# Kernel optimization log

Measured on AMD Instinct MI355X. Metric: run time of the kernel, lower is better.

Reference implementation:

```python
import jax, jax.numpy as jnp
import numpy as np

GAM1 = 1.0
GAM2 = 1.0
EPS = 0.01
NUM_CLASSES = 10


def setup_inputs() -> dict:
    key = jax.random.key(0)
    k1, k2 = jax.random.split(key)
    m, p = 262144, 64
    embed = jax.random.normal(k1, (m, p), dtype=jnp.float32)
    targets = jax.random.randint(k2, (m,), 0, NUM_CLASSES, dtype=jnp.int64)
    return {"embed": embed, "targets": targets}


def reference(embed, targets):
    m, p = embed.shape
    w = embed.T  # (p, m)
    I = jnp.eye(p, dtype=embed.dtype)

    # Discriminative term: logdet(I + gam1 * p/(m*eps) * w w^T) / 2
    scalar = p / (m * EPS)
    _, ld = jnp.linalg.slogdet(I + GAM1 * scalar * (w @ w.T))
    discrimn = ld / 2.0

    # Compressive term. pi[j] is diag(labels == j), so w @ pi[j] @ w^T is the
    # Gram over class-j columns; compute all class Grams in one einsum instead
    # of materializing (k, m, m).
    onehot = jax.nn.one_hot(targets, NUM_CLASSES, dtype=embed.dtype)  # (m, k)
    trPi = onehot.sum(axis=0) + 1e-8  # (k,) == trace(pi[j]) + 1e-8
    grams = jnp.einsum('pm,mk,qm->kpq', w, onehot, w)  # (k, p, p)
    scalars = p / (trPi * EPS)  # (k,)
    mats = I[None, :, :] + scalars[:, None, None] * grams
    _, lds = jnp.linalg.slogdet(mats)  # (k,)
    compress = jnp.sum(lds * trPi / m) / 2.0

    return GAM2 * (-discrimn) + compress
```

## Files before the change

kernel.cpp:

```cpp
#include <hip/hip_runtime.h>
#include <math.h>

#define NCLS 10
#define CHUNK 4096
#define PDIM 64
#define LDX 72
#define LDE 68

typedef short bf16x8 __attribute__((ext_vector_type(8)));
typedef float f32x4 __attribute__((ext_vector_type(4)));

__device__ __forceinline__ unsigned short bf16rn(float x) {
    unsigned u = __float_as_uint(x);
    return (unsigned short)((u + 0x7FFFu + ((u >> 16) & 1u)) >> 16);
}
__device__ __forceinline__ float bf16f(unsigned short h) {
    return __uint_as_float(((unsigned)h) << 16);
}


__global__ __launch_bounds__(256) void mcr_gram(
    const float4* __restrict__ embed4,
    const int* __restrict__ targets,
    float* __restrict__ gram,
    int* __restrict__ counts,
    int m)
{
    __shared__ unsigned short s_list[CHUNK];
    __shared__ int s_cnt;
    __shared__ unsigned short Xh[PDIM * LDX];
    __shared__ unsigned short Xl[PDIM * LDX];

    const int tid = threadIdx.x;
    const int cls = blockIdx.y;
    const int base = blockIdx.x * CHUNK;
    const int lane = tid & 63;

    if (tid == 0) s_cnt = 0;
    __syncthreads();

    const int lim = (m - base < CHUNK) ? (m - base) : CHUNK;
    for (int i = tid; i < lim; i += 256) {
        const bool match = (targets[base + i] == cls);
        const unsigned long long mk = __ballot(match);
        const int cnt = __popcll(mk);
        int wbase = 0;
        if (lane == 0 && cnt) wbase = atomicAdd(&s_cnt, cnt);
        wbase = __shfl(wbase, 0);
        if (match) {
            const int pre = __popcll(mk & ((1ull << lane) - 1ull));
            s_list[wbase + pre] = (unsigned short)i;
        }
    }
    __syncthreads();
    const int n = s_cnt;
    if (n == 0) return;
    if (tid == 0) atomicAdd(&counts[cls], n);

    const int p  = tid & 31;
    const int qA = tid >> 5;
    const int qB = qA + 8;
    const float4 z4 = make_float4(0.f, 0.f, 0.f, 0.f);

    auto load_step = [&](int s, float4& a00, float4& a01, float4& a10, float4& a11) {
        const int r0 = s * 64 + 2 * p;
        const int r1 = r0 + 1;
        if (r0 < n) {
            const size_t row = (size_t)(base + (int)s_list[r0]) * 16;
            a00 = embed4[row + qA];
            a01 = embed4[row + qB];
        } else { a00 = z4; a01 = z4; }
        if (r1 < n) {
            const size_t row = (size_t)(base + (int)s_list[r1]) * 16;
            a10 = embed4[row + qA];
            a11 = embed4[row + qB];
        } else { a10 = z4; a11 = z4; }
    };

    auto stage_write = [&](const float4& a00, const float4& a01,
                           const float4& a10, const float4& a11) {
#pragma unroll
        for (int half = 0; half < 2; ++half) {
            const float* x0 = half ? (const float*)&a01 : (const float*)&a00;
            const float* x1 = half ? (const float*)&a11 : (const float*)&a10;
            const int qq = half ? qB : qA;
#pragma unroll
            for (int j = 0; j < 4; ++j) {
                const int f = qq * 4 + j;
                const unsigned short h0 = bf16rn(x0[j]);
                const unsigned short h1 = bf16rn(x1[j]);
                const unsigned short l0 = bf16rn(x0[j] - bf16f(h0));
                const unsigned short l1 = bf16rn(x1[j] - bf16f(h1));
                *(unsigned int*)&Xh[f * LDX + 2 * p] = (unsigned)h0 | ((unsigned)h1 << 16);
                *(unsigned int*)&Xl[f * LDX + 2 * p] = (unsigned)l0 | ((unsigned)l1 << 16);
            }
        }
    };

    const int w = tid >> 6;
    const int wr = w >> 1, wc = w & 1;
    const int fb = (lane & 15) * LDX + 8 * (lane >> 4);

    f32x4 acc[4];
#pragma unroll
    for (int i = 0; i < 4; ++i) acc[i] = (f32x4){0.f, 0.f, 0.f, 0.f};

    auto mfma_step = [&]() {
#pragma unroll
        for (int kb = 0; kb < 64; kb += 32) {
            const int t0 = (2 * wr) * 16 * LDX + fb + kb;
            const int t1 = (2 * wr + 1) * 16 * LDX + fb + kb;
            const int u0 = (2 * wc) * 16 * LDX + fb + kb;
            const int u1 = (2 * wc + 1) * 16 * LDX + fb + kb;
            const bf16x8 Ah0 = *(const bf16x8*)&Xh[t0];
            const bf16x8 Ah1 = *(const bf16x8*)&Xh[t1];
            const bf16x8 Al0 = *(const bf16x8*)&Xl[t0];
            const bf16x8 Al1 = *(const bf16x8*)&Xl[t1];
            const bf16x8 Bh0 = *(const bf16x8*)&Xh[u0];
            const bf16x8 Bh1 = *(const bf16x8*)&Xh[u1];
            const bf16x8 Bl0 = *(const bf16x8*)&Xl[u0];
            const bf16x8 Bl1 = *(const bf16x8*)&Xl[u1];

            acc[0] = __builtin_amdgcn_mfma_f32_16x16x32_bf16(Ah0, Bh0, acc[0], 0, 0, 0);
            acc[1] = __builtin_amdgcn_mfma_f32_16x16x32_bf16(Ah0, Bh1, acc[1], 0, 0, 0);
            acc[2] = __builtin_amdgcn_mfma_f32_16x16x32_bf16(Ah1, Bh0, acc[2], 0, 0, 0);
            acc[3] = __builtin_amdgcn_mfma_f32_16x16x32_bf16(Ah1, Bh1, acc[3], 0, 0, 0);

            acc[0] = __builtin_amdgcn_mfma_f32_16x16x32_bf16(Ah0, Bl0, acc[0], 0, 0, 0);
            acc[1] = __builtin_amdgcn_mfma_f32_16x16x32_bf16(Ah0, Bl1, acc[1], 0, 0, 0);
            acc[2] = __builtin_amdgcn_mfma_f32_16x16x32_bf16(Ah1, Bl0, acc[2], 0, 0, 0);
            acc[3] = __builtin_amdgcn_mfma_f32_16x16x32_bf16(Ah1, Bl1, acc[3], 0, 0, 0);

            acc[0] = __builtin_amdgcn_mfma_f32_16x16x32_bf16(Al0, Bh0, acc[0], 0, 0, 0);
            acc[1] = __builtin_amdgcn_mfma_f32_16x16x32_bf16(Al0, Bh1, acc[1], 0, 0, 0);
            acc[2] = __builtin_amdgcn_mfma_f32_16x16x32_bf16(Al1, Bh0, acc[2], 0, 0, 0);
            acc[3] = __builtin_amdgcn_mfma_f32_16x16x32_bf16(Al1, Bh1, acc[3], 0, 0, 0);
        }
    };

    const int nsteps = (n + 63) >> 6;
    float4 A00, A01, A10, A11, B00, B01, B10, B11;
    load_step(0, A00, A01, A10, A11);
    load_step(1, B00, B01, B10, B11);

    for (int s = 0; s < nsteps; ++s) {
        if ((s & 1) == 0) {
            stage_write(A00, A01, A10, A11);
            load_step(s + 2, A00, A01, A10, A11);
        } else {
            stage_write(B00, B01, B10, B11);
            load_step(s + 2, B00, B01, B10, B11);
        }
        __syncthreads();
        mfma_step();
        __syncthreads();
    }

    float* gk = gram + cls * (PDIM * PDIM);
    float* gt = gram + NCLS * (PDIM * PDIM);
#pragma unroll
    for (int i1 = 0; i1 < 2; ++i1)
#pragma unroll
        for (int i2 = 0; i2 < 2; ++i2) {
            const int ar = (2 * wr + i1) * 16 + (lane >> 4) * 4;
            const int b  = (2 * wc + i2) * 16 + (lane & 15);
            const f32x4 v = acc[i1 * 2 + i2];
#pragma unroll
            for (int j = 0; j < 4; ++j) {
                const int a = ar + j;
                if (a <= b) {
                    atomicAdd(&gk[a * PDIM + b], v[j]);
                    atomicAdd(&gt[a * PDIM + b], v[j]);
                }
            }
        }
}

__device__ __forceinline__ float gU(const float* __restrict__ gram, int k, int a, int b) {
    const int lo = a < b ? a : b;
    const int hi = a < b ? b : a;
    return gram[k * (PDIM * PDIM) + lo * PDIM + hi];
}

__global__ __launch_bounds__(256) void mcr_logdet(
    const float* __restrict__ gram,
    const int* __restrict__ counts,
    double* __restrict__ contrib,
    unsigned* __restrict__ ctr,
    float* __restrict__ out,
    int m)
{
    __shared__ float E[PDIM * LDE];
    __shared__ float F[PDIM * LDE];
    __shared__ float H[PDIM * LDE];
    __shared__ float G3[PDIM * LDE];
    __shared__ double s_red[4][7];
    __shared__ double s_alpha, s_beta, s_logs, s_w;

    const int tid = threadIdx.x;
    const int k = blockIdx.x;
    const bool tot = (k == NCLS);

    if (tid < PDIM) {
        double d = (double)gU(gram, k, tid, tid);
#pragma unroll
        for (int off = 32; off > 0; off >>= 1) d += __shfl_down(d, off);
        if (tid == 0) {
            const double trG = d;
            const double denom = tot ? (double)m : ((double)counts[k] + 1e-8);
            const double c = (double)PDIM / (denom * 0.01);
            const double s = 1.0 + c * trG / (double)PDIM;
            s_alpha = c / s;
            s_beta = 1.0 / s - 1.0;
            s_logs = (double)PDIM * log(s);
            s_w = tot ? -0.5 : 0.5 * denom / (double)m;
        }
    }
    __syncthreads();

    const double alpha = s_alpha;
    const double beta = s_beta;
    const int ta = (tid >> 4) << 2;
    const int tb = (tid & 15) << 2;

#pragma unroll
    for (int i = 0; i < 4; ++i) {
        const int a = ta + i;
#pragma unroll
        for (int j = 0; j < 4; ++j) {
            const int b = tb + j;
            double v = alpha * (double)gU(gram, k, a, b);
            if (a == b) v += beta;
            E[a * LDE + b] = (float)v;
        }
    }
    __syncthreads();

    {
        float f[4][4];
#pragma unroll
        for (int i = 0; i < 4; ++i)
#pragma unroll
            for (int j = 0; j < 4; ++j) f[i][j] = 0.0f;
#pragma unroll 4
        for (int t = 0; t < PDIM; ++t) {
            const float4 ea4 = *reinterpret_cast<const float4*>(&E[t * LDE + ta]);
            const float4 eb4 = *reinterpret_cast<const float4*>(&E[t * LDE + tb]);
            const float ea[4] = {ea4.x, ea4.y, ea4.z, ea4.w};
            const float eb[4] = {eb4.x, eb4.y, eb4.z, eb4.w};
#pragma unroll
            for (int i = 0; i < 4; ++i)
#pragma unroll
                for (int j = 0; j < 4; ++j) f[i][j] = fmaf(ea[i], eb[j], f[i][j]);
        }
#pragma unroll
        for (int i = 0; i < 4; ++i)
            *reinterpret_cast<float4*>(&F[(ta + i) * LDE + tb]) =
                make_float4(f[i][0], f[i][1], f[i][2], f[i][3]);
    }
    __syncthreads();

    {
        float h[4][4], g3[4][4];
#pragma unroll
        for (int i = 0; i < 4; ++i)
#pragma unroll
            for (int j = 0; j < 4; ++j) { h[i][j] = 0.0f; g3[i][j] = 0.0f; }
#pragma unroll 4
        for (int t = 0; t < PDIM; ++t) {
            const float4 fa4 = *reinterpret_cast<const float4*>(&F[t * LDE + ta]);
            const float4 fb4 = *reinterpret_cast<const float4*>(&F[t * LDE + tb]);
            const float4 eb4 = *reinterpret_cast<const float4*>(&E[t * LDE + tb]);
            const float fa[4] = {fa4.x, fa4.y, fa4.z, fa4.w};
            const float fb[4] = {fb4.x, fb4.y, fb4.z, fb4.w};
            const float eb[4] = {eb4.x, eb4.y, eb4.z, eb4.w};
#pragma unroll
            for (int i = 0; i < 4; ++i)
#pragma unroll
                for (int j = 0; j < 4; ++j) {
                    h[i][j] = fmaf(fa[i], fb[j], h[i][j]);
                    g3[i][j] = fmaf(fa[i], eb[j], g3[i][j]);
                }
        }
#pragma unroll
        for (int i = 0; i < 4; ++i) {
            *reinterpret_cast<float4*>(&H[(ta + i) * LDE + tb]) =
                make_float4(h[i][0], h[i][1], h[i][2], h[i][3]);
            *reinterpret_cast<float4*>(&G3[(ta + i) * LDE + tb]) =
                make_float4(g3[i][0], g3[i][1], g3[i][2], g3[i][3]);
        }
    }
    __syncthreads();

    double t2 = 0, t3 = 0, t4 = 0, t5 = 0, t6 = 0, t7 = 0, t8 = 0;
#pragma unroll
    for (int i = 0; i < 4; ++i)
#pragma unroll
        for (int j = 0; j < 4; ++j) {
            const int idx = (ta + i) * LDE + tb + j;
            const double e = (double)E[idx];
            const double f = (double)F[idx];
            const double h = (double)H[idx];
            const double g = (double)G3[idx];
            t2 += e * e; t3 += f * e; t4 += f * f;
            t5 += h * e; t6 += h * f; t7 += h * g; t8 += h * h;
        }
#pragma unroll
    for (int off = 32; off > 0; off >>= 1) {
        t2 += __shfl_down(t2, off);
        t3 += __shfl_down(t3, off);
        t4 += __shfl_down(t4, off);
        t5 += __shfl_down(t5, off);
        t6 += __shfl_down(t6, off);
        t7 += __shfl_down(t7, off);
        t8 += __shfl_down(t8, off);
    }
    const int lane = tid & 63;
    const int wid = tid >> 6;
    if (lane == 0) {
        s_red[wid][0] = t2; s_red[wid][1] = t3; s_red[wid][2] = t4;
        s_red[wid][3] = t5; s_red[wid][4] = t6; s_red[wid][5] = t7;
        s_red[wid][6] = t8;
    }
    __syncthreads();
    if (tid == 0) {
        double r[7];
        for (int q = 0; q < 7; ++q) {
            r[q] = 0.0;
            for (int w = 0; w < 4; ++w) r[q] += s_red[w][q];
        }
        const double ld = s_logs
            - r[0] / 2.0 + r[1] / 3.0 - r[2] / 4.0 + r[3] / 5.0
            - r[4] / 6.0 + r[5] / 7.0 - r[6] / 8.0;
        contrib[k] = s_w * ld;
        __threadfence();
        const unsigned old = atomicAdd(ctr, 1u);
        if (old == NCLS) {
            double t = 0.0;
            for (int i = 0; i <= NCLS; ++i)
                t += atomicAdd(&contrib[i], 0.0);
            out[0] = (float)t;
        }
    }
}

extern "C" void kernel_launch(void* const* d_in, const int* in_sizes, int n_in,
                              void* d_out, int out_size, void* d_ws, size_t ws_size,
                              hipStream_t stream) {
    const float* embed = (const float*)d_in[0];
    const int* targets = (const int*)d_in[1];
    float* out = (float*)d_out;
    const int m = in_sizes[0] / PDIM;

    char* ws = (char*)d_ws;
    float* gram = (float*)ws;
    int* counts = (int*)(ws + 180224);
    unsigned* ctr = (unsigned*)(ws + 180264);
    double* contrib = (double*)(ws + 180352);

    hipMemsetAsync(ws, 0, 180268, stream);

    dim3 g1((m + CHUNK - 1) / CHUNK, NCLS);
    mcr_gram<<<g1, 256, 0, stream>>>((const float4*)embed, targets, gram, counts, m);
    mcr_logdet<<<dim3(NCLS + 1), 256, 0, stream>>>(gram, counts, contrib, ctr, out, m);
}
```

Baseline: 148.0 us.

## Give each wavefront its own 32-row staging tile and compute only upper-triangle tiles

Gram accumulation now gives each of the four wavefronts an independent 32-row batch in a private LDS staging buffer. This removes the block-wide __syncthreads pair per step. Each wave computes only the 10 upper-triangular 16x16 tiles of the full 64x64 Gram instead of splitting 4 tiles per wave over a 2x2 grid. Partial results are reduced across waves with LDS atomics before the global atomics, and CHUNK is halved to launch more blocks. The cost is more accumulator registers, redundant triangle work per wave, and the loss of explicit prefetch double-buffering.

Result: slower. 212.3 us (+43.4%).

```diff
diff --git a/kernel.cpp b/kernel.cpp
--- a/kernel.cpp
+++ b/kernel.cpp
@@ -2,9 +2,9 @@
 #include <math.h>
 
 #define NCLS 10
-#define CHUNK 4096
+#define CHUNK 2048
 #define PDIM 64
-#define LDX 72
+#define LDX2 40
 #define LDE 68
 
 typedef short bf16x8 __attribute__((ext_vector_type(8)));
@@ -17,6 +17,8 @@
 __device__ __forceinline__ float bf16f(unsigned short h) {
     return __uint_as_float(((unsigned)h) << 16);
 }
+
+#define TIDX(fi, fj) ((fi) * 4 + (fj) - ((fi) * ((fi) + 1)) / 2)
 
 
 __global__ __launch_bounds__(256) void mcr_gram(
@@ -28,13 +30,13 @@
 {
     __shared__ unsigned short s_list[CHUNK];
     __shared__ int s_cnt;
-    __shared__ unsigned short Xh[PDIM * LDX];
-    __shared__ unsigned short Xl[PDIM * LDX];
+    __shared__ alignas(16) unsigned short s_stage[4][2][PDIM * LDX2];
 
     const int tid = threadIdx.x;
     const int cls = blockIdx.y;
     const int base = blockIdx.x * CHUNK;
     const int lane = tid & 63;
+    const int w = tid >> 6;
 
     if (tid == 0) s_cnt = 0;
     __syncthreads();
@@ -57,123 +59,91 @@
     if (n == 0) return;
     if (tid == 0) atomicAdd(&counts[cls], n);
 
-    const int p  = tid & 31;
-    const int qA = tid >> 5;
-    const int qB = qA + 8;
+    const int rg = lane & 3;
+    const int q  = lane >> 2;
+    const int t16 = lane & 15;
+    const int s4  = lane >> 4;
+    unsigned short* Xh = &s_stage[w][0][0];
+    unsigned short* Xl = &s_stage[w][1][0];
     const float4 z4 = make_float4(0.f, 0.f, 0.f, 0.f);
 
-    auto load_step = [&](int s, float4& a00, float4& a01, float4& a10, float4& a11) {
-        const int r0 = s * 64 + 2 * p;
-        const int r1 = r0 + 1;
-        if (r0 < n) {
-            const size_t row = (size_t)(base + (int)s_list[r0]) * 16;
-            a00 = embed4[row + qA];
-            a01 = embed4[row + qB];
-        } else { a00 = z4; a01 = z4; }
-        if (r1 < n) {
-            const size_t row = (size_t)(base + (int)s_list[r1]) * 16;
-            a10 = embed4[row + qA];
-            a11 = embed4[row + qB];
-        } else { a10 = z4; a11 = z4; }
-    };
-
-    auto stage_write = [&](const float4& a00, const float4& a01,
-                           const float4& a10, const float4& a11) {
-#pragma unroll
-        for (int half = 0; half < 2; ++half) {
-            const float* x0 = half ? (const float*)&a01 : (const float*)&a00;
-            const float* x1 = half ? (const float*)&a11 : (const float*)&a10;
-            const int qq = half ? qB : qA;
-#pragma unroll
-            for (int j = 0; j < 4; ++j) {
-                const int f = qq * 4 + j;
-                const unsigned short h0 = bf16rn(x0[j]);
-                const unsigned short h1 = bf16rn(x1[j]);
-                const unsigned short l0 = bf16rn(x0[j] - bf16f(h0));
-                const unsigned short l1 = bf16rn(x1[j] - bf16f(h1));
-                *(unsigned int*)&Xh[f * LDX + 2 * p] = (unsigned)h0 | ((unsigned)h1 << 16);
-                *(unsigned int*)&Xl[f * LDX + 2 * p] = (unsigned)l0 | ((unsigned)l1 << 16);
+    f32x4 acc[10];
+#pragma unroll
+    for (int i = 0; i < 10; ++i) acc[i] = (f32x4){0.f, 0.f, 0.f, 0.f};
+
+    const int nb = (n + 31) >> 5;
+    for (int b = w; b < nb; b += 4) {
+        float4 v[8];
+#pragma unroll
+        for (int i = 0; i < 8; ++i) {
+            const int idx = b * 32 + 8 * rg + i;
+            if (idx < n)
+                v[i] = embed4[(size_t)(base + (int)s_list[idx]) * 16 + q];
+            else
+                v[i] = z4;
+        }
+#pragma unroll
+        for (int j = 0; j < 4; ++j) {
+            bf16x8 hv, lv;
+#pragma unroll
+            for (int i = 0; i < 8; ++i) {
+                const float x = (j == 0) ? v[i].x : (j == 1) ? v[i].y
+                              : (j == 2) ? v[i].z : v[i].w;
+                const unsigned short h = bf16rn(x);
+                hv[i] = (short)h;
+                lv[i] = (short)bf16rn(x - bf16f(h));
             }
-        }
-    };
-
-    const int w = tid >> 6;
-    const int wr = w >> 1, wc = w & 1;
-    const int fb = (lane & 15) * LDX + 8 * (lane >> 4);
-
-    f32x4 acc[4];
-#pragma unroll
-    for (int i = 0; i < 4; ++i) acc[i] = (f32x4){0.f, 0.f, 0.f, 0.f};
-
-    auto mfma_step = [&]() {
-#pragma unroll
-        for (int kb = 0; kb < 64; kb += 32) {
-            const int t0 = (2 * wr) * 16 * LDX + fb + kb;
-            const int t1 = (2 * wr + 1) * 16 * LDX + fb + kb;
-            const int u0 = (2 * wc) * 16 * LDX + fb + kb;
-            const int u1 = (2 * wc + 1) * 16 * LDX + fb + kb;
-            const bf16x8 Ah0 = *(const bf16x8*)&Xh[t0];
-            const bf16x8 Ah1 = *(const bf16x8*)&Xh[t1];
-            const bf16x8 Al0 = *(const bf16x8*)&Xl[t0];
-            const bf16x8 Al1 = *(const bf16x8*)&Xl[t1];
-            const bf16x8 Bh0 = *(const bf16x8*)&Xh[u0];
-            const bf16x8 Bh1 = *(const bf16x8*)&Xh[u1];
-            const bf16x8 Bl0 = *(const bf16x8*)&Xl[u0];
-            const bf16x8 Bl1 = *(const bf16x8*)&Xl[u1];
-
-            acc[0] = __builtin_amdgcn_mfma_f32_16x16x32_bf16(Ah0, Bh0, acc[0], 0, 0, 0);
-            acc[1] = __builtin_amdgcn_mfma_f32_16x16x32_bf16(Ah0, Bh1, acc[1], 0, 0, 0);
-            acc[2] = __builtin_amdgcn_mfma_f32_16x16x32_bf16(Ah1, Bh0, acc[2], 0, 0, 0);
-            acc[3] = __builtin_amdgcn_mfma_f32_16x16x32_bf16(Ah1, Bh1, acc[3], 0, 0, 0);
-
-            acc[0] = __builtin_amdgcn_mfma_f32_16x16x32_bf16(Ah0, Bl0, acc[0], 0, 0, 0);
-            acc[1] = __builtin_amdgcn_mfma_f32_16x16x32_bf16(Ah0, Bl1, acc[1], 0, 0, 0);
-            acc[2] = __builtin_amdgcn_mfma_f32_16x16x32_bf16(Ah1, Bl0, acc[2], 0, 0, 0);
-            acc[3] = __builtin_amdgcn_mfma_f32_16x16x32_bf16(Ah1, Bl1, acc[3], 0, 0, 0);
-
-            acc[0] = __builtin_amdgcn_mfma_f32_16x16x32_bf16(Al0, Bh0, acc[0], 0, 0, 0);
-            acc[1] = __builtin_amdgcn_mfma_f32_16x16x32_bf16(Al0, Bh1, acc[1], 0, 0, 0);
-            acc[2] = __builtin_amdgcn_mfma_f32_16x16x32_bf16(Al1, Bh0, acc[2], 0, 0, 0);
-            acc[3] = __builtin_amdgcn_mfma_f32_16x16x32_bf16(Al1, Bh1, acc[3], 0, 0, 0);
-        }
-    };
-
-    const int nsteps = (n + 63) >> 6;
-    float4 A00, A01, A10, A11, B00, B01, B10, B11;
-    load_step(0, A00, A01, A10, A11);
-    load_step(1, B00, B01, B10, B11);
-
-    for (int s = 0; s < nsteps; ++s) {
-        if ((s & 1) == 0) {
-            stage_write(A00, A01, A10, A11);
-            load_step(s + 2, A00, A01, A10, A11);
-        } else {
-            stage_write(B00, B01, B10, B11);
-            load_step(s + 2, B00, B01, B10, B11);
-        }
-        __syncthreads();
-        mfma_step();
-        __syncthreads();
-    }
+            const int f = q * 4 + j;
+            *(bf16x8*)&Xh[f * LDX2 + 8 * rg] = hv;
+            *(bf16x8*)&Xl[f * LDX2 + 8 * rg] = lv;
+        }
+        bf16x8 fh[4], fl[4];
+#pragma unroll
+        for (int fb = 0; fb < 4; ++fb) {
+            fh[fb] = *(const bf16x8*)&Xh[(fb * 16 + t16) * LDX2 + 8 * s4];
+            fl[fb] = *(const bf16x8*)&Xl[(fb * 16 + t16) * LDX2 + 8 * s4];
+        }
+#pragma unroll
+        for (int fi = 0; fi < 4; ++fi)
+#pragma unroll
+            for (int fj = fi; fj < 4; ++fj) {
+                const int t = TIDX(fi, fj);
+                acc[t] = __builtin_amdgcn_mfma_f32_16x16x32_bf16(fh[fi], fh[fj], acc[t], 0, 0, 0);
+                acc[t] = __builtin_amdgcn_mfma_f32_16x16x32_bf16(fh[fi], fl[fj], acc[t], 0, 0, 0);
+                acc[t] = __builtin_amdgcn_mfma_f32_16x16x32_bf16(fl[fi], fh[fj], acc[t], 0, 0, 0);
+            }
+    }
+
+    __syncthreads();
+    float* s_gram = (float*)&s_stage[0][0][0];
+#pragma unroll
+    for (int i = 0; i < 16; ++i) s_gram[tid + 256 * i] = 0.0f;
+    __syncthreads();
+#pragma unroll
+    for (int fi = 0; fi < 4; ++fi)
+#pragma unroll
+        for (int fj = fi; fj < 4; ++fj) {
+            const int t = TIDX(fi, fj);
+            const int a0 = fi * 16 + s4 * 4;
+            const int bc = fj * 16 + t16;
+#pragma unroll
+            for (int j = 0; j < 4; ++j)
+                atomicAdd(&s_gram[(a0 + j) * PDIM + bc], acc[t][j]);
+        }
+    __syncthreads();
 
     float* gk = gram + cls * (PDIM * PDIM);
     float* gt = gram + NCLS * (PDIM * PDIM);
 #pragma unroll
-    for (int i1 = 0; i1 < 2; ++i1)
-#pragma unroll
-        for (int i2 = 0; i2 < 2; ++i2) {
-            const int ar = (2 * wr + i1) * 16 + (lane >> 4) * 4;
-            const int b  = (2 * wc + i2) * 16 + (lane & 15);
-            const f32x4 v = acc[i1 * 2 + i2];
-#pragma unroll
-            for (int j = 0; j < 4; ++j) {
-                const int a = ar + j;
-                if (a <= b) {
-                    atomicAdd(&gk[a * PDIM + b], v[j]);
-                    atomicAdd(&gt[a * PDIM + b], v[j]);
-                }
-            }
-        }
+    for (int k = 0; k < 16; ++k) {
+        const int e = tid + 256 * k;
+        const int a = e >> 6, bc = e & 63;
+        if (a <= bc) {
+            const float val = s_gram[e];
+            atomicAdd(&gk[e], val);
+            atomicAdd(&gt[e], val);
+        }
+    }
 }
 
 __device__ __forceinline__ float gU(const float* __restrict__ gram, int k, int a, int b) {
```

## Counting-sort rows by class before Gram accumulation and derive total Gram

Applied to the files above, without the earlier changes.

Adds histogram, scan and scatter kernels that bucket row indices by class into BROWS-padded segments, so each Gram block processes exactly 512 rows of one class with a fixed unrolled loop. This replaces the per-class rescans of the targets over every chunk and the per-block compaction. The total Gram is no longer accumulated with atomics; the logdet kernel sums the ten class Grams instead. The cost is three extra kernel launches and gathers of rows spread across the whole array.

Result: slower. 180.9 us (+22.2%).

```diff
diff --git a/kernel.cpp b/kernel.cpp
--- a/kernel.cpp
+++ b/kernel.cpp
@@ -2,7 +2,8 @@
 #include <math.h>
 
 #define NCLS 10
-#define CHUNK 4096
+#define SCHUNK 2048
+#define BROWS 512
 #define PDIM 64
 #define LDX 72
 #define LDE 68
@@ -19,43 +20,104 @@
 }
 
 
+__global__ __launch_bounds__(256) void mcr_hist(
+    const int* __restrict__ targets, int* __restrict__ hist, int m, int nch)
+{
+    __shared__ int h[NCLS];
+    const int tid = threadIdx.x, c = blockIdx.x, base = c * SCHUNK;
+    if (tid < NCLS) h[tid] = 0;
+    __syncthreads();
+    const int lim = (m - base < SCHUNK) ? (m - base) : SCHUNK;
+    for (int i = tid; i < lim; i += 256) atomicAdd(&h[targets[base + i]], 1);
+    __syncthreads();
+    if (tid < NCLS) hist[tid * nch + c] = h[tid];
+}
+
+__global__ __launch_bounds__(256) void mcr_scan(
+    const int* __restrict__ hist, int* __restrict__ offs,
+    int* __restrict__ seg_start, int* __restrict__ cls_count,
+    int* __restrict__ blk_class, int* __restrict__ sorted_idx,
+    int nch, int nblk)
+{
+    __shared__ int sh[NCLS * 128];
+    __shared__ int so[NCLS * 128];
+    __shared__ int stot[NCLS];
+    __shared__ int sseg[NCLS + 1];
+    const int tid = threadIdx.x;
+    for (int i = tid; i < NCLS * nch; i += 256) sh[i] = hist[i];
+    __syncthreads();
+    if (tid < NCLS) {
+        int run = 0;
+        for (int c = 0; c < nch; ++c) { so[tid * nch + c] = run; run += sh[tid * nch + c]; }
+        stot[tid] = run;
+    }
+    __syncthreads();
+    if (tid == 0) {
+        int s = 0;
+        for (int k = 0; k < NCLS; ++k) { sseg[k] = s; s += ((stot[k] + BROWS - 1) / BROWS) * BROWS; }
+        sseg[NCLS] = s;
+    }
+    __syncthreads();
+    for (int i = tid; i < NCLS * nch; i += 256) offs[i] = sseg[i / nch] + so[i];
+    if (tid < NCLS) cls_count[tid] = stot[tid];
+    if (tid < NCLS + 1) seg_start[tid] = sseg[tid];
+    for (int b = tid; b < nblk; b += 256) {
+        const int rs = b * BROWS;
+        int k = -1;
+#pragma unroll
+        for (int j = 0; j < NCLS; ++j)
+            if (rs >= sseg[j] && rs < sseg[j + 1]) k = j;
+        blk_class[b] = k;
+    }
+#pragma unroll
+    for (int k = 0; k < NCLS; ++k) {
+        const int ps = sseg[k] + stot[k], pe = sseg[k + 1];
+        for (int j = ps + tid; j < pe; j += 256) sorted_idx[j] = -1;
+    }
+}
+
+__global__ __launch_bounds__(256) void mcr_scatter(
+    const int* __restrict__ targets, const int* __restrict__ offs,
+    int* __restrict__ sorted_idx, int m, int nch)
+{
+    __shared__ int cur[NCLS];
+    const int tid = threadIdx.x, c = blockIdx.x, base = c * SCHUNK;
+    const int lane = tid & 63;
+    if (tid < NCLS) cur[tid] = offs[tid * nch + c];
+    __syncthreads();
+    const int lim = (m - base < SCHUNK) ? (m - base) : SCHUNK;
+    for (int i = tid; i < lim; i += 256) {
+        const int t = targets[base + i];
+#pragma unroll
+        for (int k = 0; k < NCLS; ++k) {
+            const unsigned long long mk = __ballot(t == k);
+            if (mk) {
+                int wb = 0;
+                if (lane == 0) wb = atomicAdd(&cur[k], __popcll(mk));
+                wb = __shfl(wb, 0);
+                if (t == k) {
+                    const int pre = __popcll(mk & ((1ull << lane) - 1ull));
+                    sorted_idx[wb + pre] = base + i;
+                }
+            }
+        }
+    }
+}
+
 __global__ __launch_bounds__(256) void mcr_gram(
     const float4* __restrict__ embed4,
-    const int* __restrict__ targets,
-    float* __restrict__ gram,
-    int* __restrict__ counts,
-    int m)
+    const int* __restrict__ sorted_idx,
+    const int* __restrict__ blk_class,
+    float* __restrict__ gram)
 {
-    __shared__ unsigned short s_list[CHUNK];
-    __shared__ int s_cnt;
     __shared__ unsigned short Xh[PDIM * LDX];
     __shared__ unsigned short Xl[PDIM * LDX];
 
     const int tid = threadIdx.x;
-    const int cls = blockIdx.y;
-    const int base = blockIdx.x * CHUNK;
+    const int cls = blk_class[blockIdx.x];
+    if (cls < 0) return;
+    const int* __restrict__ ridx = sorted_idx + blockIdx.x * BROWS;
     const int lane = tid & 63;
-
-    if (tid == 0) s_cnt = 0;
-    __syncthreads();
-
-    const int lim = (m - base < CHUNK) ? (m - base) : CHUNK;
-    for (int i = tid; i < lim; i += 256) {
-        const bool match = (targets[base + i] == cls);
-        const unsigned long long mk = __ballot(match);
-        const int cnt = __popcll(mk);
-        int wbase = 0;
-        if (lane == 0 && cnt) wbase = atomicAdd(&s_cnt, cnt);
-        wbase = __shfl(wbase, 0);
-        if (match) {
-            const int pre = __popcll(mk & ((1ull << lane) - 1ull));
-            s_list[wbase + pre] = (unsigned short)i;
-        }
-    }
-    __syncthreads();
-    const int n = s_cnt;
-    if (n == 0) return;
-    if (tid == 0) atomicAdd(&counts[cls], n);
 
     const int p  = tid & 31;
     const int qA = tid >> 5;
@@ -64,16 +126,14 @@
 
     auto load_step = [&](int s, float4& a00, float4& a01, float4& a10, float4& a11) {
         const int r0 = s * 64 + 2 * p;
-        const int r1 = r0 + 1;
-        if (r0 < n) {
-            const size_t row = (size_t)(base + (int)s_list[r0]) * 16;
-            a00 = embed4[row + qA];
-            a01 = embed4[row + qB];
+        const int i0 = ridx[r0], i1 = ridx[r0 + 1];
+        if (i0 >= 0) {
+            a00 = embed4[(size_t)i0 * 16 + qA];
+            a01 = embed4[(size_t)i0 * 16 + qB];
         } else { a00 = z4; a01 = z4; }
-        if (r1 < n) {
-            const size_t row = (size_t)(base + (int)s_list[r1]) * 16;
-            a10 = embed4[row + qA];
-            a11 = embed4[row + qB];
+        if (i1 >= 0) {
+            a10 = embed4[(size_t)i1 * 16 + qA];
+            a11 = embed4[(size_t)i1 * 16 + qB];
         } else { a10 = z4; a11 = z4; }
     };
 
@@ -138,18 +198,18 @@
         }
     };
 
-    const int nsteps = (n + 63) >> 6;
     float4 A00, A01, A10, A11, B00, B01, B10, B11;
     load_step(0, A00, A01, A10, A11);
     load_step(1, B00, B01, B10, B11);
 
-    for (int s = 0; s < nsteps; ++s) {
+#pragma unroll
+    for (int s = 0; s < 8; ++s) {
         if ((s & 1) == 0) {
             stage_write(A00, A01, A10, A11);
-            load_step(s + 2, A00, A01, A10, A11);
+            if (s + 2 < 8) load_step(s + 2, A00, A01, A10, A11);
         } else {
             stage_write(B00, B01, B10, B11);
-            load_step(s + 2, B00, B01, B10, B11);
+            if (s + 2 < 8) load_step(s + 2, B00, B01, B10, B11);
         }
         __syncthreads();
         mfma_step();
@@ -157,7 +217,6 @@
     }
 
     float* gk = gram + cls * (PDIM * PDIM);
-    float* gt = gram + NCLS * (PDIM * PDIM);
 #pragma unroll
     for (int i1 = 0; i1 < 2; ++i1)
 #pragma unroll
@@ -168,10 +227,7 @@
 #pragma unroll
             for (int j = 0; j < 4; ++j) {
                 const int a = ar + j;
-                if (a <= b) {
-                    atomicAdd(&gk[a * PDIM + b], v[j]);
-                    atomicAdd(&gt[a * PDIM + b], v[j]);
-                }
+                if (a <= b) atomicAdd(&gk[a * PDIM + b], v[j]);
             }
         }
 }
@@ -181,10 +237,17 @@
     const int hi = a < b ? b : a;
     return gram[k * (PDIM * PDIM) + lo * PDIM + hi];
 }
+__device__ __forceinline__ float gT(const float* __restrict__ gram, int k, int a, int b) {
+    if (k < NCLS) return gU(gram, k, a, b);
+    float s = 0.0f;
+#pragma unroll
+    for (int c = 0; c < NCLS; ++c) s += gU(gram, c, a, b);
+    return s;
+}
 
 __global__ __launch_bounds__(256) void mcr_logdet(
     const float* __restrict__ gram,
-    const int* __restrict__ counts,
+    const int* __restrict__ cls_count,
     double* __restrict__ contrib,
     unsigned* __restrict__ ctr,
     float* __restrict__ out,
@@ -202,12 +265,12 @@
     const bool tot = (k == NCLS);
 
     if (tid < PDIM) {
-        double d = (double)gU(gram, k, tid, tid);
+        double d = (double)gT(gram, k, tid, tid);
 #pragma unroll
         for (int off = 32; off > 0; off >>= 1) d += __shfl_down(d, off);
         if (tid == 0) {
             const double trG = d;
-            const double denom = tot ? (double)m : ((double)counts[k] + 1e-8);
+            const double denom = tot ? (double)m : ((double)cls_count[k] + 1e-8);
             const double c = (double)PDIM / (denom * 0.01);
             const double s = 1.0 + c * trG / (double)PDIM;
             s_alpha = c / s;
@@ -229,7 +292,7 @@
 #pragma unroll
         for (int j = 0; j < 4; ++j) {
             const int b = tb + j;
-            double v = alpha * (double)gU(gram, k, a, b);
+            double v = alpha * (double)gT(gram, k, a, b);
             if (a == b) v += beta;
             E[a * LDE + b] = (float)v;
         }
@@ -351,16 +414,26 @@
     const int* targets = (const int*)d_in[1];
     float* out = (float*)d_out;
     const int m = in_sizes[0] / PDIM;
+    const int nch = (m + SCHUNK - 1) / SCHUNK;
+    const int nblk = m / BROWS + NCLS;
 
     char* ws = (char*)d_ws;
-    float* gram = (float*)ws;
-    int* counts = (int*)(ws + 180224);
-    unsigned* ctr = (unsigned*)(ws + 180264);
-    double* contrib = (double*)(ws + 180352);
-
-    hipMemsetAsync(ws, 0, 180268, stream);
-
-    dim3 g1((m + CHUNK - 1) / CHUNK, NCLS);
-    mcr_gram<<<g1, 256, 0, stream>>>((const float4*)embed, targets, gram, counts, m);
-    mcr_logdet<<<dim3(NCLS + 1), 256, 0, stream>>>(gram, counts, contrib, ctr, out, m);
-}
+    float* gram      = (float*)ws;
+    unsigned* ctr    = (unsigned*)(ws + 163840);
+    double* contrib  = (double*)(ws + 163848);
+    int* hist        = (int*)(ws + 163936);
+    int* offs        = (int*)(ws + 169056);
+    int* cls_count   = (int*)(ws + 174176);
+    int* seg_start   = (int*)(ws + 174216);
+    int* blk_class   = (int*)(ws + 174260);
+    int* sorted_idx  = (int*)(ws + 176352);
+
+    hipMemsetAsync(ws, 0, 163844, stream);
+
+    mcr_hist<<<nch, 256, 0, stream>>>(targets, hist, m, nch);
+    mcr_scan<<<1, 256, 0, stream>>>(hist, offs, seg_start, cls_count,
+                                    blk_class, sorted_idx, nch, nblk);
+    mcr_scatter<<<nch, 256, 0, stream>>>(targets, offs, sorted_idx, m, nch);
+    mcr_gram<<<nblk, 256, 0, stream>>>((const float4*)embed, sorted_idx, blk_class, gram);
+    mcr_logdet<<<NCLS + 1, 256, 0, stream>>>(gram, cls_count, contrib, ctr, out, m);
+}
```
